# Optimization experiments

Hardware: AMD Instinct MI355X
Metric: run time of the kernel (lower is better)

The kernel has to match this reference:

```python
import jax, jax.numpy as jnp
import numpy as np

HEADS = 4
HEAD_DIM = 128  # GATConv out_channels
NEG_SLOPE_ATT = 0.2   # GATConv internal leaky relu
NEG_SLOPE_ACT = 0.01  # nn.LeakyReLU() default


def gat_conv(x, edge_index, W, att_src, att_dst, bias):
    # x: [N, F]; edge_index: [2, E] (row 0 = src j, row 1 = dst i)
    N = x.shape[0]
    h = (x @ W).reshape(N, HEADS, HEAD_DIM)            # [N, H, C]
    loops = jnp.arange(N, dtype=edge_index.dtype)
    src = jnp.concatenate([edge_index[0], loops])      # add self loops
    dst = jnp.concatenate([edge_index[1], loops])
    a_src = jnp.einsum('nhc,hc->nh', h, att_src)       # [N, H]
    a_dst = jnp.einsum('nhc,hc->nh', h, att_dst)
    e = jax.nn.leaky_relu(a_src[src] + a_dst[dst], NEG_SLOPE_ATT)  # [E', H]
    # segment softmax over incoming edges of each dst node
    emax = jax.ops.segment_max(e, dst, num_segments=N)
    ex = jnp.exp(e - emax[dst])
    denom = jax.ops.segment_sum(ex, dst, num_segments=N)
    alpha = ex / (denom[dst] + 1e-16)                  # [E', H]
    msg = h[src] * alpha[:, :, None]                   # [E', H, C]
    out = jax.ops.segment_sum(msg, dst, num_segments=N)
    return out.reshape(N, HEADS * HEAD_DIM) + bias     # [N, H*C]


def branch(x, edge_index, W, att_src, att_dst, bias, fc1_w, fc1_b):
    h = gat_conv(x, edge_index, W, att_src, att_dst, bias)
    h = jax.nn.leaky_relu(h, NEG_SLOPE_ACT)
    g = jnp.mean(h, axis=0, keepdims=True)             # global mean pool, batch all zeros -> [1, H*C]
    g = jax.nn.leaky_relu(g @ fc1_w + fc1_b, NEG_SLOPE_ACT)
    return g  # dropout is identity in eval mode


def setup_inputs() -> dict:
    key = jax.random.key(0)
    ks = jax.random.split(key, 10)
    N, E, F = 20000, 320000, 512
    HC = HEADS * HEAD_DIM
    s = 1.0 / np.sqrt(F)
    return {
        'x': jax.random.normal(ks[0], (N, F), jnp.float32),
        'adj': jax.random.randint(ks[1], (2, E), 0, N, jnp.int64),
        'wt_x': jax.random.normal(ks[2], (N, F), jnp.float32),
        'wt_adj': jax.random.randint(ks[3], (2, E), 0, N, jnp.int64),
        'W': jax.random.normal(ks[4], (F, HC), jnp.float32) * s,
        'att_src': jax.random.normal(ks[5], (HEADS, HEAD_DIM), jnp.float32) * s,
        'att_dst': jax.random.normal(ks[6], (HEADS, HEAD_DIM), jnp.float32) * s,
        'bias': jnp.zeros((HC,), jnp.float32),
        'fc1_w': jax.random.normal(ks[7], (HC, 512), jnp.float32) * (1.0 / np.sqrt(HC)),
        'fc1_b': jnp.zeros((512,), jnp.float32),
    }


def reference(x, adj, wt_x, wt_adj, W, att_src, att_dst, bias, fc1_w, fc1_b):
    g = branch(x, adj, W, att_src, att_dst, bias, fc1_w, fc1_b)
    wt_g = branch(wt_x, wt_adj, W, att_src, att_dst, bias, fc1_w, fc1_b)
    xd = g - wt_g
    return jnp.concatenate([g, wt_g, xd], axis=1)  # [1, 3*512]
```

## Files before the change

### kernel.cpp

```cpp
#include <hip/hip_runtime.h>
#include <hip/hip_bf16.h>

typedef unsigned short u16;
typedef short bf16x8 __attribute__((ext_vector_type(8)));
typedef float f32x4 __attribute__((ext_vector_type(4)));
typedef float f32x2 __attribute__((ext_vector_type(2)));

__device__ __forceinline__ u16 f2b(float f) {
    unsigned x = __float_as_uint(f);
    return (u16)((x + 0x7fffu + ((x >> 16) & 1u)) >> 16);
}

__device__ __forceinline__ int pkbf(float lo, float hi) {
    return __builtin_amdgcn_perm(__float_as_uint(hi), __float_as_uint(lo), 0x07060302);
}

__device__ __forceinline__ void pkfma(f32x2& acc, f32x2 f, f32x2 ex) {
    asm("v_pk_fma_f32 %0, %1, %2, %0" : "+v"(acc) : "v"(f), "v"(ex));
}

__global__ __launch_bounds__(256) void cast_wt_kernel(const float* __restrict__ W,
                                                      u16* __restrict__ Wt) {
    __shared__ u16 tile[64][65];
    int tx = threadIdx.x & 63, ty = threadIdx.x >> 6;
    int bx = blockIdx.x & 7, by = blockIdx.x >> 3;
#pragma unroll
    for (int r = 0; r < 16; ++r) {
        int row = ty + (r << 2);
        tile[tx][row] = f2b(W[(by * 64 + row) * 512 + bx * 64 + tx]);
    }
    __syncthreads();
#pragma unroll
    for (int r = 0; r < 16; ++r) {
        int row = ty + (r << 2);
        Wt[(bx * 64 + row) * 512 + by * 64 + tx] = tile[row][tx];
    }
}

__global__ __launch_bounds__(256, 2) void gemm_fused6(
    const float* __restrict__ xA, const float* __restrict__ xW, const u16* __restrict__ Bt,
    unsigned char* __restrict__ h8, const float* __restrict__ att_src,
    const float* __restrict__ att_dst, float* __restrict__ asrc, float* __restrict__ adst,
    int N, int Mpad) {
    __shared__ float lA[2][64 * 32];
    __shared__ u16 lB[2][512 * 32];
    const int tid = threadIdx.x;
    const int w = tid >> 6, l = tid & 63;
    const int row0 = blockIdx.x * 64;
    const int head = w;
    const int mlane = l & 15, quad = l >> 4;
    const int R2v = 2 * Mpad;

    const float* src = (row0 >= Mpad) ? xW : xA;
    const int rbase = row0 - (row0 >= Mpad ? Mpad : 0);
    const int arow = (l >> 3);
    const int acol = (((l & 7) ^ arow) << 2);
    const int brow = (l >> 2);
    const int bcol = (((l & 3) ^ ((l >> 3) & 3)) << 3);

    auto stage = [&](int b, int k0) {
#pragma unroll
        for (int g = 0; g < 2; ++g) {
            int lrow = rbase + (w << 4) + (g << 3) + arow;
            lrow = min(lrow, N - 1);
            const float* ga = src + (size_t)lrow * 512 + k0 + acol;
            float* la = &lA[b][((w << 4) + (g << 3)) << 5];
            __builtin_amdgcn_global_load_lds((const __attribute__((address_space(1))) void*)ga,
                                             (__attribute__((address_space(3))) void*)la, 16, 0, 0);
        }
#pragma unroll
        for (int s = 0; s < 8; ++s) {
            const u16* gb = Bt + (size_t)((w << 7) + (s << 4) + brow) * 512 + (k0 + bcol);
            u16* lb = &lB[b][((w << 7) + (s << 4)) << 5];
            __builtin_amdgcn_global_load_lds((const __attribute__((address_space(1))) void*)gb,
                                             (__attribute__((address_space(3))) void*)lb, 16, 0, 0);
        }
    };

    f32x4 acc[4][8];
#pragma unroll
    for (int i = 0; i < 4; i++)
#pragma unroll
        for (int j = 0; j < 8; j++) acc[i][j] = f32x4{0.f, 0.f, 0.f, 0.f};

    stage(0, 0);
    __syncthreads();
    int cur = 0;
    for (int t = 0; t < 16; ++t) {
        if (t < 15) stage(cur ^ 1, (t + 1) << 5);
        bf16x8 af[4], bfr[8];
#pragma unroll
        for (int i = 0; i < 4; i++) {
            const float* rb = &lA[cur][(i * 16 + mlane) * 32];
            float4 f0 = *(const float4*)(rb + (((quad * 2) ^ (mlane & 7)) << 2));
            float4 f1 = *(const float4*)(rb + (((quad * 2 + 1) ^ (mlane & 7)) << 2));
            int* ai = (int*)&af[i];
            ai[0] = pkbf(f0.x, f0.y);
            ai[1] = pkbf(f0.z, f0.w);
            ai[2] = pkbf(f1.x, f1.y);
            ai[3] = pkbf(f1.z, f1.w);
        }
#pragma unroll
        for (int j = 0; j < 8; j++)
            bfr[j] = *(const bf16x8*)&lB[cur][((w << 7) + j * 16 + mlane) * 32 +
                                             ((quad ^ ((mlane >> 1) & 3)) << 3)];
#pragma unroll
        for (int i = 0; i < 4; i++)
#pragma unroll
            for (int j = 0; j < 8; j++)
                acc[i][j] = __builtin_amdgcn_mfma_f32_16x16x32_bf16(af[i], bfr[j], acc[i][j], 0, 0, 0);
        __syncthreads();
        cur ^= 1;
    }

    float as_j[8], ad_j[8];
#pragma unroll
    for (int j = 0; j < 8; j++) {
        as_j[j] = att_src[(head << 7) + j * 16 + mlane];
        ad_j[j] = att_dst[(head << 7) + j * 16 + mlane];
    }
#pragma unroll
    for (int i = 0; i < 4; i++) {
#pragma unroll
        for (int r = 0; r < 4; r++) {
            float vs = 0.f, vd = 0.f;
#pragma unroll
            for (int j = 0; j < 8; j++) {
                float hv = acc[i][j][r];
                vs += hv * as_j[j];
                vd += hv * ad_j[j];
            }
#pragma unroll
            for (int o = 8; o >= 1; o >>= 1) {
                vs += __shfl_xor(vs, o);
                vd += __shfl_xor(vd, o);
            }
            if (mlane == 0) {
                int rg = row0 + i * 16 + quad * 4 + r;
                asrc[head * R2v + rg] = vs;
                adst[head * R2v + rg] = vd;
            }
        }
    }

    unsigned char* hstage = (unsigned char*)&lB[0][0];
#pragma unroll
    for (int i = 0; i < 4; i++)
#pragma unroll
        for (int j = 0; j < 8; j++)
#pragma unroll
            for (int r = 0; r < 4; r++) {
                int row = i * 16 + quad * 4 + r;
                int colb = (w << 7) + j * 16 + mlane;
                float v = acc[i][j][r];
                unsigned pk = __builtin_amdgcn_cvt_pk_fp8_f32(v, v, 0, false);
                hstage[row * 512 + (colb ^ ((row & 7) << 4))] = (unsigned char)(pk & 0xff);
            }
    __syncthreads();
#pragma unroll
    for (int k = 0; k < 8; ++k) {
        int c = (k << 8) + tid;
        int hd = c >> 9;
        int rem = c & 511;
        int row = rem >> 3;
        int cch = rem & 7;
        int lofs = row * 512 + ((((hd << 7) + (cch << 4))) ^ ((row & 7) << 4));
        int4 v = *(const int4*)&hstage[lofs];
        *(int4*)&h8[(((size_t)(hd * R2v + row0 + row)) << 7) + (cch << 4)] = v;
    }
}

__global__ void csr_count(const int* __restrict__ adj, const int* __restrict__ wadj,
                          int E, int Mpad, int* __restrict__ deg) {
    int i = blockIdx.x * blockDim.x + threadIdx.x;
    if (i < 2 * E) {
        int d = (i < E) ? adj[E + i] : (wadj[E + (i - E)] + Mpad);
        atomicAdd(&deg[d], 1);
    }
}

__global__ __launch_bounds__(256) void scanA(const int* __restrict__ deg, int* __restrict__ off,
                                             int* __restrict__ bsum, int n, int N, int Mpad) {
    __shared__ int wsum[4];
    int tid = threadIdx.x, lane = tid & 63, wid = tid >> 6;
    int i = blockIdx.x * 256 + tid;
    int valid = (i < N) || (i >= Mpad && i < Mpad + N);
    int d = (i < n) ? deg[i] + (valid ? 1 : 0) : 0;
    int x = d;
#pragma unroll
    for (int o = 1; o < 64; o <<= 1) {
        int y = __shfl_up(x, (unsigned)o, 64);
        if (lane >= o) x += y;
    }
    if (lane == 63) wsum[wid] = x;
    __syncthreads();
    int woff = 0;
    for (int j = 0; j < wid; ++j) woff += wsum[j];
    if (i < n) off[i] = woff + x - d;
    if (tid == 255) bsum[blockIdx.x] = woff + x;
}

__global__ __launch_bounds__(256) void scanB(const int* __restrict__ bsum, int* __restrict__ bbase,
                                             int nb, int* __restrict__ off, int n) {
    __shared__ int wsum[4];
    int tid = threadIdx.x, lane = tid & 63, wid = tid >> 6;
    int d = (tid < nb) ? bsum[tid] : 0;
    int x = d;
#pragma unroll
    for (int o = 1; o < 64; o <<= 1) {
        int y = __shfl_up(x, (unsigned)o, 64);
        if (lane >= o) x += y;
    }
    if (lane == 63) wsum[wid] = x;
    __syncthreads();
    int woff = 0;
    for (int j = 0; j < wid; ++j) woff += wsum[j];
    int excl = woff + x - d;
    if (tid < nb) bbase[tid] = excl;
    if (tid == nb - 1) off[n] = excl + d;
}

__global__ void scanC(int* __restrict__ off, const int* __restrict__ bbase,
                      int* __restrict__ cursor, int* __restrict__ csrc, int n, int N, int Mpad) {
    int i = blockIdx.x * blockDim.x + threadIdx.x;
    if (i < n) {
        int o = off[i] + bbase[i >> 8];
        off[i] = o;
        int valid = (i < N) || (i >= Mpad && i < Mpad + N);
        if (valid) csrc[o] = i;
        cursor[i] = o + valid;
    }
}

__global__ void csr_scatter(const int* __restrict__ adj, const int* __restrict__ wadj,
                            int E, int Mpad, int* __restrict__ cursor, int* __restrict__ csrc) {
    int i = blockIdx.x * blockDim.x + threadIdx.x;
    if (i < 2 * E) {
        int s, d;
        if (i < E) {
            s = adj[i];
            d = adj[E + i];
        } else {
            s = wadj[i - E] + Mpad;
            d = wadj[E + (i - E)] + Mpad;
        }
        int p = atomicAdd(&cursor[d], 1);
        csrc[p] = s;
    }
}

__global__ __launch_bounds__(256, 6) void gat_aggregate13(
    const unsigned char* __restrict__ h8, const float* __restrict__ asrc,
    const float* __restrict__ adst, const int* __restrict__ off, const int* __restrict__ csrc,
    const float* __restrict__ bias, float* __restrict__ partAB, int Mpad) {
    const int R2 = 2 * Mpad;
    __shared__ float spool[128];
    int tid = threadIdx.x;
    if (tid < 128) spool[tid] = 0.f;
    __syncthreads();
    const int wv = tid >> 6, l = tid & 63;
    const int gi = (l >> 3) & 3;
    const int hi = l >> 5;
    const int chb = (l & 7) << 4;
    const int head = (blockIdx.x & 7) >> 1;
    const int gc = blockIdx.x & 1;
    const unsigned char* h8h = h8 + (((size_t)head * R2) << 7);
    const float* ash = asrc + (size_t)head * R2;
    const float* adh = adst + (size_t)head * R2;
    float bb[16];
#pragma unroll
    for (int k = 0; k < 16; ++k) bb[k] = bias[head * 128 + chb + k];
    float pool[16];
#pragma unroll
    for (int k = 0; k < 16; ++k) pool[k] = 0.f;

    const int hb = gc * Mpad;
    const int half = Mpad >> 1;
    int widx = ((blockIdx.x >> 3) << 2) + wv;
    const int cstride = gridDim.x >> 1;

    for (int p = widx; p < half; p += cstride) {
        int d0 = (p << 1) + hb;
        int q0 = off[d0], q1 = off[d0 + 1], q2 = off[d0 + 2];
        int n0 = q1 - q0, n1 = q2 - q1;
        int nmax = max(n0, n1);
        if (nmax == 0) continue;
        int nm = hi ? n1 : n0;
        int qm = hi ? q1 : q0;
        float ad = adh[d0 + hi];
        f32x2 acc2[8];
#pragma unroll
        for (int j = 0; j < 8; ++j) acc2[j] = f32x2{0.f, 0.f};
        float dsum = 0.f;

        int i0 = gi, i1 = 4 + gi, i2 = 8 + gi, i3 = 12 + gi;
        int E0 = csrc[qm + ((i0 < nm) ? i0 : 0)];
        int E1 = csrc[qm + ((i1 < nm) ? i1 : 0)];
        int E2 = csrc[qm + ((i2 < nm) ? i2 : 0)];
        int E3 = csrc[qm + ((i3 < nm) ? i3 : 0)];
        float A0 = ash[E0];
        int4 H0 = *(const int4*)(h8h + (((size_t)E0) << 7) + chb);
        float A1 = ash[E1];
        int4 H1 = *(const int4*)(h8h + (((size_t)E1) << 7) + chb);

#pragma unroll 2
        for (int base = 0; base < nmax; base += 4) {
            int i4 = base + 16 + gi;
            int E4 = csrc[qm + ((i4 < nm) ? i4 : 0)];
            float A2 = ash[E2];
            int4 H2 = *(const int4*)(h8h + (((size_t)E2) << 7) + chb);
            float e = A0 + ad;
            float em = fmaxf(e, 0.2f * e);
            float ex = __expf(em);
            ex = ((base + gi) < nm) ? ex : 0.f;
            dsum += ex;
            f32x2 exv = {ex, ex};
            f32x2 f;
            f = __builtin_amdgcn_cvt_pk_f32_fp8(H0.x, false); pkfma(acc2[0], f, exv);
            f = __builtin_amdgcn_cvt_pk_f32_fp8(H0.x, true);  pkfma(acc2[1], f, exv);
            f = __builtin_amdgcn_cvt_pk_f32_fp8(H0.y, false); pkfma(acc2[2], f, exv);
            f = __builtin_amdgcn_cvt_pk_f32_fp8(H0.y, true);  pkfma(acc2[3], f, exv);
            f = __builtin_amdgcn_cvt_pk_f32_fp8(H0.z, false); pkfma(acc2[4], f, exv);
            f = __builtin_amdgcn_cvt_pk_f32_fp8(H0.z, true);  pkfma(acc2[5], f, exv);
            f = __builtin_amdgcn_cvt_pk_f32_fp8(H0.w, false); pkfma(acc2[6], f, exv);
            f = __builtin_amdgcn_cvt_pk_f32_fp8(H0.w, true);  pkfma(acc2[7], f, exv);
            A0 = A1; H0 = H1;
            A1 = A2; H1 = H2;
            E2 = E3; E3 = E4;
        }
        dsum += __shfl_xor(dsum, 8);
        dsum += __shfl_xor(dsum, 16);
#pragma unroll
        for (int j = 0; j < 8; ++j) {
            acc2[j].x += __shfl_xor(acc2[j].x, 8);
            acc2[j].y += __shfl_xor(acc2[j].y, 8);
            acc2[j].x += __shfl_xor(acc2[j].x, 16);
            acc2[j].y += __shfl_xor(acc2[j].y, 16);
        }
        if (nm > 0) {
            float inv = 1.f / (dsum + 1e-16f);
#pragma unroll
            for (int j = 0; j < 8; ++j) {
                float o0 = acc2[j].x * inv + bb[2 * j];
                float o1 = acc2[j].y * inv + bb[2 * j + 1];
                pool[2 * j] += fmaxf(o0, 0.01f * o0);
                pool[2 * j + 1] += fmaxf(o1, 0.01f * o1);
            }
        }
    }
    if ((l & 31) < 8) {
#pragma unroll
        for (int k = 0; k < 16; ++k) atomicAdd(&spool[chb + k], pool[k]);
    }
    __syncthreads();
    if (tid < 128) {
        int slot = (blockIdx.x >> 3) & 63;
        float* dp = partAB + (gc ? 64 * 512 : 0) + (slot << 9) + head * 128 + tid;
        atomicAdd(dp, spool[tid]);
    }
}

__global__ __launch_bounds__(256) void fc_final2(
    const float* __restrict__ partAB, const float* __restrict__ w, const float* __restrict__ b,
    float* __restrict__ out, float invN) {
    __shared__ float gA[512], gB[512];
    __shared__ float rA[256], rB[256];
    int t = threadIdx.x;
    for (int i = t; i < 512; i += 256) {
        float sA = 0.f, sB = 0.f;
        for (int r = 0; r < 64; ++r) {
            sA += partAB[r * 512 + i];
            sB += partAB[64 * 512 + r * 512 + i];
        }
        gA[i] = sA * invN;
        gB[i] = sB * invN;
    }
    __syncthreads();
    int jj = t & 31, ks = t >> 5;
    int j = blockIdx.x * 32 + jj;
    float sA = 0.f, sB = 0.f;
    for (int k = ks * 64; k < ks * 64 + 64; ++k) {
        float wv = w[k * 512 + j];
        sA += gA[k] * wv;
        sB += gB[k] * wv;
    }
    rA[t] = sA;
    rB[t] = sB;
    __syncthreads();
    if (ks == 0) {
#pragma unroll
        for (int s2 = 1; s2 < 8; ++s2) {
            sA += rA[jj + 32 * s2];
            sB += rB[jj + 32 * s2];
        }
        sA += b[j];
        sB += b[j];
        sA = sA >= 0.f ? sA : 0.01f * sA;
        sB = sB >= 0.f ? sB : 0.01f * sB;
        out[j] = sA;
        out[512 + j] = sB;
        out[1024 + j] = sA - sB;
    }
}

extern "C" void kernel_launch(void* const* d_in, const int* in_sizes, int n_in,
                              void* d_out, int out_size, void* d_ws, size_t ws_size,
                              hipStream_t stream) {
    const float* x = (const float*)d_in[0];
    const int* adj = (const int*)d_in[1];
    const float* wtx = (const float*)d_in[2];
    const int* wadj = (const int*)d_in[3];
    const float* W = (const float*)d_in[4];
    const float* att_s = (const float*)d_in[5];
    const float* att_d = (const float*)d_in[6];
    const float* bias = (const float*)d_in[7];
    const float* fc1w = (const float*)d_in[8];
    const float* fc1b = (const float*)d_in[9];
    float* out = (float*)d_out;

    const int N = in_sizes[0] / 512;
    const int E = in_sizes[1] / 2;
    const int Mpad = ((N + 127) / 128) * 128;
    const int R2 = 2 * Mpad;
    const int nb = (R2 + 255) / 256;

    char* p = (char*)d_ws;
    auto alloc = [&](size_t bytes) -> char* {
        char* r = p;
        p += (bytes + 255) & ~(size_t)255;
        return r;
    };
    unsigned char* h8 = (unsigned char*)alloc((size_t)R2 * 512);
    u16* Wt = (u16*)alloc(512 * 512 * 2);
    float* asrc = (float*)alloc((size_t)R2 * 4 * 4);
    float* adst = (float*)alloc((size_t)R2 * 4 * 4);
    int* deg = (int*)alloc((size_t)R2 * 4);
    int* off = (int*)alloc((size_t)(R2 + 1) * 4);
    int* cursor = (int*)alloc((size_t)R2 * 4);
    int* bsum = (int*)alloc(256 * 4);
    int* bbase = (int*)alloc(256 * 4);
    int* csrc = (int*)alloc((size_t)2 * (E + N) * 4);
    float* partAB = (float*)alloc((size_t)2 * 64 * 512 * 4);

    hipMemsetAsync(partAB, 0, (size_t)2 * 64 * 512 * 4, stream);
    hipMemsetAsync(deg, 0, (size_t)R2 * 4, stream);
    cast_wt_kernel<<<64, 256, 0, stream>>>(W, Wt);

    csr_count<<<(2 * E + 255) / 256, 256, 0, stream>>>(adj, wadj, E, Mpad, deg);
    scanA<<<nb, 256, 0, stream>>>(deg, off, bsum, R2, N, Mpad);
    scanB<<<1, 256, 0, stream>>>(bsum, bbase, nb, off, R2);
    scanC<<<nb, 256, 0, stream>>>(off, bbase, cursor, csrc, R2, N, Mpad);
    csr_scatter<<<(2 * E + 255) / 256, 256, 0, stream>>>(adj, wadj, E, Mpad, cursor, csrc);

    gemm_fused6<<<R2 / 64, 256, 0, stream>>>(x, wtx, Wt, h8, att_s, att_d, asrc, adst, N, Mpad);

    gat_aggregate13<<<1536, 256, 0, stream>>>(h8, asrc, adst, off, csrc, bias, partAB, Mpad);

    fc_final2<<<16, 256, 0, stream>>>(partAB, fc1w, fc1b, out, 1.0f / (float)N);
}
```

Baseline: 326.6 us.

## Fuse memsets into cast kernel, single-block scan, raise aggregate occupancy

Zeroing of deg and partAB moves from two hipMemsetAsync calls into the weight-cast kernel. The three-kernel scan is replaced by one 1024-thread block that holds the whole degree array in LDS. The aggregate kernel's occupancy hint goes from 6 to 8 and its grid from 1536 to 2048 blocks. Together these cut launch count and per-launch overhead, but the single-block scan serializes about 40K elements and the larger grid may change how the aggregate work is split.

```diff
diff --git a/kernel.cpp b/kernel.cpp
--- a/kernel.cpp
+++ b/kernel.cpp
@@ -20,10 +20,15 @@
 }
 
 __global__ __launch_bounds__(256) void cast_wt_kernel(const float* __restrict__ W,
-                                                      u16* __restrict__ Wt) {
+                                                      u16* __restrict__ Wt,
+                                                      int* __restrict__ deg,
+                                                      float* __restrict__ partAB, int R2) {
     __shared__ u16 tile[64][65];
     int tx = threadIdx.x & 63, ty = threadIdx.x >> 6;
     int bx = blockIdx.x & 7, by = blockIdx.x >> 3;
+    int gid = blockIdx.x * 256 + threadIdx.x;
+    for (int i = gid; i < R2; i += 16384) deg[i] = 0;
+    for (int i = gid; i < 2 * 64 * 512; i += 16384) partAB[i] = 0.f;
 #pragma unroll
     for (int r = 0; r < 16; ++r) {
         int row = ty + (r << 2);
@@ -179,14 +184,27 @@
     }
 }
 
-__global__ __launch_bounds__(256) void scanA(const int* __restrict__ deg, int* __restrict__ off,
-                                             int* __restrict__ bsum, int n, int N, int Mpad) {
-    __shared__ int wsum[4];
-    int tid = threadIdx.x, lane = tid & 63, wid = tid >> 6;
-    int i = blockIdx.x * 256 + tid;
-    int valid = (i < N) || (i >= Mpad && i < Mpad + N);
-    int d = (i < n) ? deg[i] + (valid ? 1 : 0) : 0;
-    int x = d;
+__global__ __launch_bounds__(1024) void scan_fused(
+    const int* __restrict__ deg, int* __restrict__ off, int* __restrict__ cursor,
+    int* __restrict__ csrc, int n, int N, int Mpad) {
+    __shared__ int s[40192];
+    __shared__ int wsum[16];
+    __shared__ int stotal;
+    const int t = threadIdx.x;
+    const int lane = t & 63, wid = t >> 6;
+    for (int i = t; i < n; i += 1024) {
+        int valid = (i < N) || (i >= Mpad && i < Mpad + N);
+        s[i] = deg[i] + valid;
+    }
+    __syncthreads();
+    const int base = t * 40;
+    int sum = 0;
+#pragma unroll 4
+    for (int j = 0; j < 40; ++j) {
+        int i = base + j;
+        if (i < n) sum += s[i];
+    }
+    int x = sum;
 #pragma unroll
     for (int o = 1; o < 64; o <<= 1) {
         int y = __shfl_up(x, (unsigned)o, 64);
@@ -196,40 +214,27 @@
     __syncthreads();
     int woff = 0;
     for (int j = 0; j < wid; ++j) woff += wsum[j];
-    if (i < n) off[i] = woff + x - d;
-    if (tid == 255) bsum[blockIdx.x] = woff + x;
-}
-
-__global__ __launch_bounds__(256) void scanB(const int* __restrict__ bsum, int* __restrict__ bbase,
-                                             int nb, int* __restrict__ off, int n) {
-    __shared__ int wsum[4];
-    int tid = threadIdx.x, lane = tid & 63, wid = tid >> 6;
-    int d = (tid < nb) ? bsum[tid] : 0;
-    int x = d;
-#pragma unroll
-    for (int o = 1; o < 64; o <<= 1) {
-        int y = __shfl_up(x, (unsigned)o, 64);
-        if (lane >= o) x += y;
-    }
-    if (lane == 63) wsum[wid] = x;
-    __syncthreads();
-    int woff = 0;
-    for (int j = 0; j < wid; ++j) woff += wsum[j];
-    int excl = woff + x - d;
-    if (tid < nb) bbase[tid] = excl;
-    if (tid == nb - 1) off[n] = excl + d;
-}
-
-__global__ void scanC(int* __restrict__ off, const int* __restrict__ bbase,
-                      int* __restrict__ cursor, int* __restrict__ csrc, int n, int N, int Mpad) {
-    int i = blockIdx.x * blockDim.x + threadIdx.x;
-    if (i < n) {
-        int o = off[i] + bbase[i >> 8];
+    int excl = woff + x - sum;
+    if (t == 1023) stotal = excl + sum;
+    int run = excl;
+#pragma unroll 4
+    for (int j = 0; j < 40; ++j) {
+        int i = base + j;
+        if (i < n) {
+            int d = s[i];
+            s[i] = run;
+            run += d;
+        }
+    }
+    __syncthreads();
+    for (int i = t; i < n; i += 1024) {
+        int o = s[i];
+        int valid = (i < N) || (i >= Mpad && i < Mpad + N);
         off[i] = o;
-        int valid = (i < N) || (i >= Mpad && i < Mpad + N);
+        cursor[i] = o + valid;
         if (valid) csrc[o] = i;
-        cursor[i] = o + valid;
-    }
+    }
+    if (t == 0) off[n] = stotal;
 }
 
 __global__ void csr_scatter(const int* __restrict__ adj, const int* __restrict__ wadj,
@@ -249,7 +254,7 @@
     }
 }
 
-__global__ __launch_bounds__(256, 6) void gat_aggregate13(
+__global__ __launch_bounds__(256, 8) void gat_aggregate14(
     const unsigned char* __restrict__ h8, const float* __restrict__ asrc,
     const float* __restrict__ adst, const int* __restrict__ off, const int* __restrict__ csrc,
     const float* __restrict__ bias, float* __restrict__ partAB, int Mpad) {
@@ -422,7 +427,6 @@
     const int E = in_sizes[1] / 2;
     const int Mpad = ((N + 127) / 128) * 128;
     const int R2 = 2 * Mpad;
-    const int nb = (R2 + 255) / 256;
 
     char* p = (char*)d_ws;
     auto alloc = [&](size_t bytes) -> char* {
@@ -437,24 +441,18 @@
     int* deg = (int*)alloc((size_t)R2 * 4);
     int* off = (int*)alloc((size_t)(R2 + 1) * 4);
     int* cursor = (int*)alloc((size_t)R2 * 4);
-    int* bsum = (int*)alloc(256 * 4);
-    int* bbase = (int*)alloc(256 * 4);
     int* csrc = (int*)alloc((size_t)2 * (E + N) * 4);
     float* partAB = (float*)alloc((size_t)2 * 64 * 512 * 4);
 
-    hipMemsetAsync(partAB, 0, (size_t)2 * 64 * 512 * 4, stream);
-    hipMemsetAsync(deg, 0, (size_t)R2 * 4, stream);
-    cast_wt_kernel<<<64, 256, 0, stream>>>(W, Wt);
+    cast_wt_kernel<<<64, 256, 0, stream>>>(W, Wt, deg, partAB, R2);
 
     csr_count<<<(2 * E + 255) / 256, 256, 0, stream>>>(adj, wadj, E, Mpad, deg);
-    scanA<<<nb, 256, 0, stream>>>(deg, off, bsum, R2, N, Mpad);
-    scanB<<<1, 256, 0, stream>>>(bsum, bbase, nb, off, R2);
-    scanC<<<nb, 256, 0, stream>>>(off, bbase, cursor, csrc, R2, N, Mpad);
+    scan_fused<<<1, 1024, 0, stream>>>(deg, off, cursor, csrc, R2, N, Mpad);
     csr_scatter<<<(2 * E + 255) / 256, 256, 0, stream>>>(adj, wadj, E, Mpad, cursor, csrc);
 
     gemm_fused6<<<R2 / 64, 256, 0, stream>>>(x, wtx, Wt, h8, att_s, att_d, asrc, adst, N, Mpad);
 
-    gat_aggregate13<<<1536, 256, 0, stream>>>(h8, asrc, adst, off, csrc, bias, partAB, Mpad);
+    gat_aggregate14<<<2048, 256, 0, stream>>>(h8, asrc, adst, off, csrc, bias, partAB, Mpad);
 
     fc_final2<<<16, 256, 0, stream>>>(partAB, fc1w, fc1b, out, 1.0f / (float)N);
 }
```

Result: slower. 382.2 us (+17.0%).
